# Optimization experiments

Measured on AMD Instinct MI355X. Metric: run time of the kernel, lower is better.

## Reference

```python
import jax, jax.numpy as jnp
import numpy as np

DT = 0.1

def setup_inputs() -> dict:
    key = jax.random.key(0)
    ks = jax.random.split(key, 11)
    B, I, H = 65536, 128, 256
    return {
        "x": jax.random.normal(ks[0], (B, I), jnp.float32),
        "prev_input": jax.random.normal(ks[1], (B, I), jnp.float32),
        "hidden": jax.random.normal(ks[2], (B, H), jnp.float32),
        "W_in_w": jax.random.normal(ks[3], (H, I), jnp.float32) * 0.05,
        "W_in_b": jax.random.normal(ks[4], (H,), jnp.float32) * 0.05,
        "W_rec_w": jax.random.normal(ks[5], (H, H), jnp.float32) * 0.05,
        "W_rec_b": jax.random.normal(ks[6], (H,), jnp.float32) * 0.05,
        "attn_w": jax.random.normal(ks[7], (H, H), jnp.float32) * 0.05,
        "attn_b": jax.random.normal(ks[8], (H,), jnp.float32) * 0.05,
        "ev_w": jax.random.normal(ks[9], (1, 2 * I), jnp.float32) * 0.05,
        "ev_b": jax.random.normal(ks[10], (1,), jnp.float32) * 0.05,
        "tau": jnp.ones((H,), jnp.float32),
    }

def reference(x, prev_input, hidden, W_in_w, W_in_b, W_rec_w, W_rec_b,
              attn_w, attn_b, ev_w, ev_b, tau):
    # event detection from concatenated current + previous input
    event_input = jnp.concatenate([x, prev_input], axis=1)  # (B, 2I)
    event_weight = jax.nn.sigmoid(event_input @ ev_w.T + ev_b)  # (B, 1)
    # liquid dynamics
    input_contrib = jnp.tanh(x @ W_in_w.T + W_in_b)  # (B, H)
    attention_weights = jax.nn.sigmoid(hidden @ attn_w.T + attn_b)  # (B, H)
    recurrent_contrib = jnp.tanh((hidden * attention_weights) @ W_rec_w.T + W_rec_b)
    tau_clamped = jnp.clip(tau, 0.1, 10.0)  # (H,)
    dhidden_dt = (-hidden + input_contrib + recurrent_contrib) / tau_clamped
    new_hidden = hidden + DT * dhidden_dt * (1.0 + event_weight)
    return new_hidden, event_weight
```

## Files before the change

kernel.cpp:

```cpp
#include <hip/hip_runtime.h>

#define BI 128
#define BH 256
#define MT 32
#define NT 256

using f32x4  = __attribute__((ext_vector_type(4))) float;
using short8 = __attribute__((ext_vector_type(8))) short;

__device__ __forceinline__ unsigned short f2bf(float f) {
  unsigned u = __float_as_uint(f);
  u = (u + 0x7FFFu + ((u >> 16) & 1u)) >> 16;
  return (unsigned short)u;
}
__device__ __forceinline__ float bf2f(unsigned short h) {
  return __uint_as_float(((unsigned)h) << 16);
}
__device__ __forceinline__ float fast_tanh(float v) {
  return 1.f - 2.f / (1.f + __expf(2.f * v));
}
__device__ __forceinline__ float fast_sigmoid(float v) {
  return 1.f / (1.f + __expf(-v));
}

__global__ void pack_w(const float* __restrict__ W, unsigned short* __restrict__ dst,
                       int K, int total) {
  int t = blockIdx.x * blockDim.x + threadIdx.x;
  if (t >= total) return;
  int lane = t & 63;
  int tile = t >> 6;
  int KT = K >> 5;
  int nf = tile / KT, kt = tile - nf * KT;
  int n  = nf * 16 + (lane & 15);
  int k0 = kt * 32 + (lane >> 4) * 8;
  const float* src = W + (size_t)n * K + k0;
#pragma unroll
  for (int j = 0; j < 8; ++j) dst[(size_t)t * 8 + j] = f2bf(src[j]);
}

__global__ __launch_bounds__(NT, 3) void ha_kernel(
    const float* __restrict__ hidden, const float* __restrict__ attn_b,
    const unsigned short* __restrict__ attn_p,
    unsigned short* __restrict__ ha_out) {
  extern __shared__ char smem[];
  const int tid = threadIdx.x;
  const int lane = tid & 63;
  const int wid = tid >> 6;
  const int r0 = blockIdx.x * MT;
  const int lrow = lane & 15;
  const int lk = lane >> 4;

#pragma unroll
  for (int it = 0; it < 8; ++it) {
    int idx4 = it * NT + tid;
    int row = idx4 >> 6;
    int c = idx4 & 63;
    f32x4 v = *(const f32x4*)(hidden + (size_t)(r0 + row) * BH + c * 4);
    unsigned h01 = (unsigned)f2bf(v[0]) | ((unsigned)f2bf(v[1]) << 16);
    unsigned h23 = (unsigned)f2bf(v[2]) | ((unsigned)f2bf(v[3]) << 16);
    *(unsigned long long*)(smem + row * 512 + ((c * 8) ^ ((row & 7) << 4))) =
        (unsigned long long)h01 | ((unsigned long long)h23 << 32);
  }
  __syncthreads();

  f32x4 acc[2][4] = {};
  {
    const short8* bW = (const short8*)attn_p;
#pragma unroll
    for (int kt = 0; kt < 8; ++kt) {
      short8 ah[2];
#pragma unroll
      for (int mf = 0; mf < 2; ++mf) {
        int row = mf * 16 + lrow;
        ah[mf] = *(const short8*)(smem + row * 512 + ((kt * 64 + lk * 16) ^ ((row & 7) << 4)));
      }
#pragma unroll
      for (int nf = 0; nf < 4; ++nf) {
        short8 b = bW[((wid * 4 + nf) * 8 + kt) * 64 + lane];
#pragma unroll
        for (int mf = 0; mf < 2; ++mf)
          acc[mf][nf] = __builtin_amdgcn_mfma_f32_16x16x32_bf16(ah[mf], b, acc[mf][nf], 0, 0, 0);
      }
    }
  }

#pragma unroll
  for (int nf = 0; nf < 4; ++nf) {
    int col = wid * 64 + nf * 16 + lrow;
    float bb = attn_b[col];
#pragma unroll
    for (int mf = 0; mf < 2; ++mf) {
#pragma unroll
      for (int j = 0; j < 4; ++j) {
        int row = mf * 16 + lk * 4 + j;
        float aw = fast_sigmoid(acc[mf][nf][j] + bb);
        int hoff = row * 512 + ((col * 2) ^ ((row & 7) << 4));
        float h = bf2f(*(const unsigned short*)(smem + hoff));
        *(unsigned short*)(smem + 16384 + hoff) = f2bf(h * aw);
      }
    }
  }
  __syncthreads();

#pragma unroll
  for (int p = 0; p < 4; ++p) {
    int c = p * NT + tid;
    int row = c >> 5;
    int cp = (c & 31) * 16;
    f32x4 v = *(const f32x4*)(smem + 16384 + row * 512 + (cp ^ ((row & 7) << 4)));
    *(f32x4*)((char*)ha_out + (size_t)blockIdx.x * 16384 + (size_t)c * 16) = v;
  }
}

__global__ __launch_bounds__(NT, 3) void ic_kernel(
    const float* __restrict__ x, const float* __restrict__ prev,
    const float* __restrict__ w_in_b,
    const float* __restrict__ ev_w, const float* __restrict__ ev_b,
    const unsigned short* __restrict__ win_p,
    float* __restrict__ out, int Bn) {
  extern __shared__ char smem[];
  const int tid = threadIdx.x;
  const int lane = tid & 63;
  const int wid = tid >> 6;
  const int r0 = blockIdx.x * MT;
  const int lrow = lane & 15;
  const int lk = lane >> 4;

#pragma unroll
  for (int it = 0; it < 4; ++it) {
    int idx4 = it * NT + tid;
    int row = idx4 >> 5;
    int c = idx4 & 31;
    f32x4 v = *(const f32x4*)(x + (size_t)(r0 + row) * BI + c * 4);
    unsigned h01 = (unsigned)f2bf(v[0]) | ((unsigned)f2bf(v[1]) << 16);
    unsigned h23 = (unsigned)f2bf(v[2]) | ((unsigned)f2bf(v[3]) << 16);
    *(unsigned long long*)(smem + row * 256 + ((c * 8) ^ ((row & 7) << 4))) =
        (unsigned long long)h01 | ((unsigned long long)h23 << 32);
  }

  {
    int r = tid >> 3, p = tid & 7;
    float s = 0.f;
    const float* src = (p < 4) ? (x + (size_t)(r0 + r) * BI + p * 32)
                               : (prev + (size_t)(r0 + r) * BI + (p - 4) * 32);
    const float* wr = ev_w + p * 32;
#pragma unroll
    for (int i = 0; i < 8; ++i) {
      f32x4 a = *(const f32x4*)(src + i * 4);
      f32x4 w = *(const f32x4*)(wr + i * 4);
      s += a[0] * w[0] + a[1] * w[1] + a[2] * w[2] + a[3] * w[3];
    }
    s += __shfl_xor(s, 1);
    s += __shfl_xor(s, 2);
    s += __shfl_xor(s, 4);
    if (p == 0)
      out[(size_t)Bn * BH + r0 + r] = fast_sigmoid(s + ev_b[0]);
  }
  __syncthreads();

  f32x4 ic[2][4] = {};
  {
    const short8* bW = (const short8*)win_p;
#pragma unroll
    for (int kt = 0; kt < 4; ++kt) {
      short8 ax[2];
#pragma unroll
      for (int mf = 0; mf < 2; ++mf) {
        int row = mf * 16 + lrow;
        ax[mf] = *(const short8*)(smem + row * 256 + ((kt * 64 + lk * 16) ^ ((row & 7) << 4)));
      }
#pragma unroll
      for (int nf = 0; nf < 4; ++nf) {
        short8 b = bW[((wid * 4 + nf) * 4 + kt) * 64 + lane];
#pragma unroll
        for (int mf = 0; mf < 2; ++mf)
          ic[mf][nf] = __builtin_amdgcn_mfma_f32_16x16x32_bf16(ax[mf], b, ic[mf][nf], 0, 0, 0);
      }
    }
  }

#pragma unroll
  for (int nf = 0; nf < 4; ++nf) {
    int col = wid * 64 + nf * 16 + lrow;
    float bb = w_in_b[col];
#pragma unroll
    for (int mf = 0; mf < 2; ++mf) {
#pragma unroll
      for (int j = 0; j < 4; ++j) {
        int row = mf * 16 + lk * 4 + j;
        *(float*)(smem + 8192 + row * 1024 + ((col * 4) ^ ((row & 7) << 4))) =
            fast_tanh(ic[mf][nf][j] + bb);
      }
    }
  }
  __syncthreads();

#pragma unroll
  for (int it = 0; it < 8; ++it) {
    int row = it * 4 + wid;
    f32x4 v = *(const f32x4*)(smem + 8192 + row * 1024 + ((lane * 16) ^ ((row & 7) << 4)));
    *(f32x4*)(out + (size_t)(r0 + row) * BH + lane * 4) = v;
  }
}

__global__ __launch_bounds__(NT, 3) void rec_kernel(
    const float* __restrict__ hidden, const float* __restrict__ w_rec_b,
    const float* __restrict__ tau,
    const unsigned short* __restrict__ wrec_p,
    const unsigned short* __restrict__ ha_in,
    float* __restrict__ out, int Bn) {
  extern __shared__ char smem[];
  const int tid = threadIdx.x;
  const int lane = tid & 63;
  const int wid = tid >> 6;
  const int r0 = blockIdx.x * MT;
  const int lrow = lane & 15;
  const int lk = lane >> 4;

#pragma unroll
  for (int p = 0; p < 4; ++p) {
    int c = p * NT + tid;
    int row = c >> 5;
    int cp = (c & 31) * 16;
    f32x4 v = *(const f32x4*)((const char*)ha_in + (size_t)blockIdx.x * 16384 + (size_t)c * 16);
    *(f32x4*)(smem + row * 512 + (cp ^ ((row & 7) << 4))) = v;
  }
  __syncthreads();

  f32x4 rcc[2][4] = {};
  {
    const short8* bW = (const short8*)wrec_p;
#pragma unroll
    for (int kt = 0; kt < 8; ++kt) {
      short8 ah[2];
#pragma unroll
      for (int mf = 0; mf < 2; ++mf) {
        int row = mf * 16 + lrow;
        ah[mf] = *(const short8*)(smem + row * 512 + ((kt * 64 + lk * 16) ^ ((row & 7) << 4)));
      }
#pragma unroll
      for (int nf = 0; nf < 4; ++nf) {
        short8 b = bW[((wid * 4 + nf) * 8 + kt) * 64 + lane];
#pragma unroll
        for (int mf = 0; mf < 2; ++mf)
          rcc[mf][nf] = __builtin_amdgcn_mfma_f32_16x16x32_bf16(ah[mf], b, rcc[mf][nf], 0, 0, 0);
      }
    }
  }

#pragma unroll
  for (int nf = 0; nf < 4; ++nf) {
    int col = wid * 64 + nf * 16 + lrow;
    float brec = w_rec_b[col];
#pragma unroll
    for (int mf = 0; mf < 2; ++mf) {
#pragma unroll
      for (int j = 0; j < 4; ++j) {
        int row = mf * 16 + lk * 4 + j;
        *(float*)(smem + 16384 + row * 1024 + ((col * 4) ^ ((row & 7) << 4))) =
            fast_tanh(rcc[mf][nf][j] + brec);
      }
    }
  }
  __syncthreads();

  {
    f32x4 t4 = *(const f32x4*)(tau + lane * 4);
    f32x4 dtt;
#pragma unroll
    for (int i = 0; i < 4; ++i) {
      float t = fminf(fmaxf(t4[i], 0.1f), 10.f);
      dtt[i] = 0.1f / t;
    }
#pragma unroll
    for (int it = 0; it < 8; ++it) {
      int row = it * 4 + wid;
      float e1 = 1.f + out[(size_t)Bn * BH + r0 + row];
      f32x4 s4 = *(const f32x4*)(smem + 16384 + row * 1024 + ((lane * 16) ^ ((row & 7) << 4)));
      float* orow = out + (size_t)(r0 + row) * BH + lane * 4;
      f32x4 ic4 = *(const f32x4*)orow;
      f32x4 h4 = *(const f32x4*)(hidden + (size_t)(r0 + row) * BH + lane * 4);
      f32x4 o;
#pragma unroll
      for (int i = 0; i < 4; ++i)
        o[i] = h4[i] + dtt[i] * (ic4[i] + s4[i] - h4[i]) * e1;
      *(f32x4*)orow = o;
    }
  }
}

extern "C" void kernel_launch(void* const* d_in, const int* in_sizes, int n_in,
                              void* d_out, int out_size, void* d_ws, size_t ws_size,
                              hipStream_t stream) {
  const float* x       = (const float*)d_in[0];
  const float* prev    = (const float*)d_in[1];
  const float* hidden  = (const float*)d_in[2];
  const float* W_in_w  = (const float*)d_in[3];
  const float* W_in_b  = (const float*)d_in[4];
  const float* W_rec_w = (const float*)d_in[5];
  const float* W_rec_b = (const float*)d_in[6];
  const float* attn_w  = (const float*)d_in[7];
  const float* attn_b  = (const float*)d_in[8];
  const float* ev_w    = (const float*)d_in[9];
  const float* ev_b    = (const float*)d_in[10];
  const float* tau     = (const float*)d_in[11];
  int Bn = in_sizes[0] / BI;

  unsigned short* ws = (unsigned short*)d_ws;
  unsigned short* win_p  = ws;
  unsigned short* attn_p = ws + 32768;
  unsigned short* wrec_p = ws + 98304;
  unsigned short* ha_ws  = ws + 163840;

  pack_w<<<(4096 + 255) / 256, 256, 0, stream>>>(W_in_w, win_p, BI, 4096);
  pack_w<<<(8192 + 255) / 256, 256, 0, stream>>>(attn_w, attn_p, BH, 8192);
  pack_w<<<(8192 + 255) / 256, 256, 0, stream>>>(W_rec_w, wrec_p, BH, 8192);

  ha_kernel<<<Bn / MT, NT, 32768, stream>>>(hidden, attn_b, attn_p, ha_ws);

  ic_kernel<<<Bn / MT, NT, 40960, stream>>>(
      x, prev, W_in_b, ev_w, ev_b, win_p, (float*)d_out, Bn);

  rec_kernel<<<Bn / MT, NT, 49152, stream>>>(
      hidden, W_rec_b, tau, wrec_p, ha_ws, (float*)d_out, Bn);
}
```

Before: 121.7 us.

## Store input contribution as bf16 in output scratch and split event weight kernel

The event-weight computation moves out of ic_kernel into its own kernel. ic_kernel now writes its tanh input contribution as packed bf16 tiles into the first half of each block's output region, which halves that intermediate traffic. rec_kernel prefetches those bf16 values into registers before it overwrites the same region with the final fp32 result, and an explicit vmcnt wait guards the ordering. The costs are an extra kernel launch, bf16 rounding of the input contribution, and reliance on each block reading its own region before writing it.

```diff
diff --git a/kernel.cpp b/kernel.cpp
--- a/kernel.cpp
+++ b/kernel.cpp
@@ -38,6 +38,30 @@
   for (int j = 0; j < 8; ++j) dst[(size_t)t * 8 + j] = f2bf(src[j]);
 }
 
+__global__ __launch_bounds__(NT, 4) void ew_kernel(
+    const float* __restrict__ x, const float* __restrict__ prev,
+    const float* __restrict__ ev_w, const float* __restrict__ ev_b,
+    float* __restrict__ out, int Bn) {
+  const int tid = threadIdx.x;
+  const int r0 = blockIdx.x * MT;
+  int r = tid >> 3, p = tid & 7;
+  float s = 0.f;
+  const float* src = (p < 4) ? (x + (size_t)(r0 + r) * BI + p * 32)
+                             : (prev + (size_t)(r0 + r) * BI + (p - 4) * 32);
+  const float* wr = ev_w + p * 32;
+#pragma unroll
+  for (int i = 0; i < 8; ++i) {
+    f32x4 a = *(const f32x4*)(src + i * 4);
+    f32x4 w = *(const f32x4*)(wr + i * 4);
+    s += a[0] * w[0] + a[1] * w[1] + a[2] * w[2] + a[3] * w[3];
+  }
+  s += __shfl_xor(s, 1);
+  s += __shfl_xor(s, 2);
+  s += __shfl_xor(s, 4);
+  if (p == 0)
+    out[(size_t)Bn * BH + r0 + r] = fast_sigmoid(s + ev_b[0]);
+}
+
 __global__ __launch_bounds__(NT, 3) void ha_kernel(
     const float* __restrict__ hidden, const float* __restrict__ attn_b,
     const unsigned short* __restrict__ attn_p,
@@ -113,11 +137,9 @@
 }
 
 __global__ __launch_bounds__(NT, 3) void ic_kernel(
-    const float* __restrict__ x, const float* __restrict__ prev,
-    const float* __restrict__ w_in_b,
-    const float* __restrict__ ev_w, const float* __restrict__ ev_b,
+    const float* __restrict__ x, const float* __restrict__ w_in_b,
     const unsigned short* __restrict__ win_p,
-    float* __restrict__ out, int Bn) {
+    float* __restrict__ out) {
   extern __shared__ char smem[];
   const int tid = threadIdx.x;
   const int lane = tid & 63;
@@ -137,25 +159,6 @@
     *(unsigned long long*)(smem + row * 256 + ((c * 8) ^ ((row & 7) << 4))) =
         (unsigned long long)h01 | ((unsigned long long)h23 << 32);
   }
-
-  {
-    int r = tid >> 3, p = tid & 7;
-    float s = 0.f;
-    const float* src = (p < 4) ? (x + (size_t)(r0 + r) * BI + p * 32)
-                               : (prev + (size_t)(r0 + r) * BI + (p - 4) * 32);
-    const float* wr = ev_w + p * 32;
-#pragma unroll
-    for (int i = 0; i < 8; ++i) {
-      f32x4 a = *(const f32x4*)(src + i * 4);
-      f32x4 w = *(const f32x4*)(wr + i * 4);
-      s += a[0] * w[0] + a[1] * w[1] + a[2] * w[2] + a[3] * w[3];
-    }
-    s += __shfl_xor(s, 1);
-    s += __shfl_xor(s, 2);
-    s += __shfl_xor(s, 4);
-    if (p == 0)
-      out[(size_t)Bn * BH + r0 + r] = fast_sigmoid(s + ev_b[0]);
-  }
   __syncthreads();
 
   f32x4 ic[2][4] = {};
@@ -188,18 +191,20 @@
 #pragma unroll
       for (int j = 0; j < 4; ++j) {
         int row = mf * 16 + lk * 4 + j;
-        *(float*)(smem + 8192 + row * 1024 + ((col * 4) ^ ((row & 7) << 4))) =
-            fast_tanh(ic[mf][nf][j] + bb);
-      }
-    }
-  }
-  __syncthreads();
-
-#pragma unroll
-  for (int it = 0; it < 8; ++it) {
-    int row = it * 4 + wid;
-    f32x4 v = *(const f32x4*)(smem + 8192 + row * 1024 + ((lane * 16) ^ ((row & 7) << 4)));
-    *(f32x4*)(out + (size_t)(r0 + row) * BH + lane * 4) = v;
+        *(unsigned short*)(smem + 8192 + row * 512 + ((col * 2) ^ ((row & 7) << 4))) =
+            f2bf(fast_tanh(ic[mf][nf][j] + bb));
+      }
+    }
+  }
+  __syncthreads();
+
+#pragma unroll
+  for (int p = 0; p < 4; ++p) {
+    int c = p * NT + tid;
+    int row = c >> 5;
+    int cp = (c & 31) * 16;
+    f32x4 v = *(const f32x4*)(smem + 8192 + row * 512 + (cp ^ ((row & 7) << 4)));
+    *(f32x4*)((char*)out + (size_t)blockIdx.x * 32768 + (size_t)c * 16) = v;
   }
 }
 
@@ -217,6 +222,14 @@
   const int lrow = lane & 15;
   const int lk = lane >> 4;
 
+  unsigned long long icp[8];
+  {
+    const char* icbase = (const char*)out + (size_t)blockIdx.x * 32768;
+#pragma unroll
+    for (int it = 0; it < 8; ++it)
+      icp[it] = *(const unsigned long long*)(icbase + (it * 4 + wid) * 512 + lane * 8);
+  }
+
 #pragma unroll
   for (int p = 0; p < 4; ++p) {
     int c = p * NT + tid;
@@ -262,6 +275,7 @@
       }
     }
   }
+  asm volatile("s_waitcnt vmcnt(0)" ::: "memory");
   __syncthreads();
 
   {
@@ -277,14 +291,14 @@
       int row = it * 4 + wid;
       float e1 = 1.f + out[(size_t)Bn * BH + r0 + row];
       f32x4 s4 = *(const f32x4*)(smem + 16384 + row * 1024 + ((lane * 16) ^ ((row & 7) << 4)));
-      float* orow = out + (size_t)(r0 + row) * BH + lane * 4;
-      f32x4 ic4 = *(const f32x4*)orow;
       f32x4 h4 = *(const f32x4*)(hidden + (size_t)(r0 + row) * BH + lane * 4);
       f32x4 o;
 #pragma unroll
-      for (int i = 0; i < 4; ++i)
-        o[i] = h4[i] + dtt[i] * (ic4[i] + s4[i] - h4[i]) * e1;
-      *(f32x4*)orow = o;
+      for (int i = 0; i < 4; ++i) {
+        float icv = bf2f((unsigned short)(icp[it] >> (16 * i)));
+        o[i] = h4[i] + dtt[i] * (icv + s4[i] - h4[i]) * e1;
+      }
+      *(f32x4*)(out + (size_t)(r0 + row) * BH + lane * 4) = o;
     }
   }
 }
@@ -316,10 +330,11 @@
   pack_w<<<(8192 + 255) / 256, 256, 0, stream>>>(attn_w, attn_p, BH, 8192);
   pack_w<<<(8192 + 255) / 256, 256, 0, stream>>>(W_rec_w, wrec_p, BH, 8192);
 
+  ew_kernel<<<Bn / MT, NT, 0, stream>>>(x, prev, ev_w, ev_b, (float*)d_out, Bn);
+
   ha_kernel<<<Bn / MT, NT, 32768, stream>>>(hidden, attn_b, attn_p, ha_ws);
 
-  ic_kernel<<<Bn / MT, NT, 40960, stream>>>(
-      x, prev, W_in_b, ev_w, ev_b, win_p, (float*)d_out, Bn);
+  ic_kernel<<<Bn / MT, NT, 24576, stream>>>(x, W_in_b, win_p, (float*)d_out);
 
   rec_kernel<<<Bn / MT, NT, 49152, stream>>>(
       hidden, W_rec_b, tau, wrec_p, ha_ws, (float*)d_out, Bn);
```

New measurement: 123.3 us. About the same (+1.3%).
